# Optimization experiments

Hardware: AMD Instinct MI355X
Metric: run time of the kernel (lower is better)

Reference implementation:

```python
import jax, jax.numpy as jnp
import numpy as np

DIM = 2048
H = 16        # num query heads
HK = 2        # num kv heads
D = DIM // H  # head_dim = 128
G = H // HK   # q heads per kv head = 8
SCALE = 1.0 / np.sqrt(D)


def setup_inputs() -> dict:
    key = jax.random.key(0)
    ks = jax.random.split(key, 9)
    xavier = lambda k, fi, fo: jax.random.uniform(k, (fi, fo), jnp.float32,
                                                  -np.sqrt(6.0 / (fi + fo)), np.sqrt(6.0 / (fi + fo)))
    return {
        "x": jax.random.normal(ks[0], (2, 2048, DIM), jnp.float32),
        "Wq": xavier(ks[1], DIM, H * D),  "bq": jnp.zeros((H * D,), jnp.float32),
        "Wk": xavier(ks[2], DIM, HK * D), "bk": jnp.zeros((HK * D,), jnp.float32),
        "Wv": xavier(ks[3], DIM, HK * D), "bv": jnp.zeros((HK * D,), jnp.float32),
        "Wo": xavier(ks[4], H * D, DIM),  "bo": jnp.zeros((DIM,), jnp.float32),
    }


def reference(x, Wq, bq, Wk, bk, Wv, bv, Wo, bo):
    B, T, C = x.shape
    # projections; q grouped as (kv_head, group) so repeat_interleave becomes a broadcast
    q = (x @ Wq + bq).reshape(B, T, HK, G, D)   # [B,T,Hk,G,D]
    k = (x @ Wk + bk).reshape(B, T, HK, D)      # [B,T,Hk,D]
    v = (x @ Wv + bv).reshape(B, T, HK, D)
    # scores: [B,Hk,G,Tq,Tk] — shared K broadcast across the G query heads per kv head
    scores = jnp.einsum('bqhgd,bshd->bhgqs', q, k) * SCALE
    scores = jnp.clip(scores, -100.0, 100.0)
    attn = jax.nn.softmax(scores, axis=-1)
    out = jnp.einsum('bhgqs,bshd->bqhgd', attn, v).reshape(B, T, H * D)
    return out @ Wo + bo
```

## Files before the change

kernel.cpp:

```cpp
#include <hip/hip_runtime.h>
#include <cstdint>

typedef __bf16 bf16x8 __attribute__((ext_vector_type(8)));
typedef float floatx4 __attribute__((ext_vector_type(4)));
typedef unsigned short u16;
typedef unsigned int u32;

#define SCALE2 0.1275434297677098f
#define CLIP2  144.26950408889634f

__device__ __forceinline__ u16 f2bf(float f) {
  union { float f; u32 i; } v; v.f = f;
  u32 r = v.i + 0x7fffu + ((v.i >> 16) & 1u);
  return (u16)(r >> 16);
}

__device__ __forceinline__ void gll16(const void* g, void* l) {
  __builtin_amdgcn_global_load_lds(
      (const __attribute__((address_space(1))) u32*)g,
      (__attribute__((address_space(3))) u32*)l, 16, 0, 0);
}

__global__ __launch_bounds__(256) void convert_bf16(
    const float* __restrict__ src, u16* __restrict__ dst, int n4) {
  int i = blockIdx.x * 256 + threadIdx.x;
  if (i >= n4) return;
  float4 v = ((const float4*)src)[i];
  ushort4 o;
  o.x = f2bf(v.x); o.y = f2bf(v.y); o.z = f2bf(v.z); o.w = f2bf(v.w);
  ((ushort4*)dst)[i] = o;
}

__global__ __launch_bounds__(256) void transpose_cat(
    const float* __restrict__ W0, const float* __restrict__ W1,
    const float* __restrict__ W2,
    int n1, int n2, int ld0, int ld1, int ld2, int K, u16* __restrict__ Bt) {
  __shared__ u16 tile[32][33];
  const int k0 = blockIdx.x * 32, n0 = blockIdx.y * 32;
  const float* src; int ld, nb;
  if (n0 < n1)      { src = W0; ld = ld0; nb = n0; }
  else if (n0 < n2) { src = W1; ld = ld1; nb = n0 - n1; }
  else              { src = W2; ld = ld2; nb = n0 - n2; }
  const int tx = threadIdx.x, ty = threadIdx.y;
#pragma unroll
  for (int i = 0; i < 4; i++) {
    int k = ty + i * 8;
    tile[k][tx] = f2bf(src[(size_t)(k0 + k) * ld + nb + tx]);
  }
  __syncthreads();
#pragma unroll
  for (int i = 0; i < 4; i++) {
    int n = ty + i * 8;
    Bt[(size_t)(n0 + n) * K + k0 + tx] = tile[tx][n];
  }
}

template <int EPI>
__global__ __launch_bounds__(256) void gemm_bt(
    const u16* __restrict__ A, const u16* __restrict__ Bt,
    const float* __restrict__ bias0, const float* __restrict__ bias1,
    const float* __restrict__ bias2,
    u16* __restrict__ out0, u16* __restrict__ out1, u16* __restrict__ out2,
    float* __restrict__ outf,
    int M, int N, int K) {
  __shared__ u16 As[2][128][32];
  __shared__ u16 Bs[2][128][32];
  const int tid  = threadIdx.x;
  const int w    = tid >> 6, L = tid & 63, ln = L & 15, quad = L >> 4;
  const int m0   = blockIdx.y * 128, n0 = blockIdx.x * 128;
  const int mw   = (w & 1) * 64, nw = (w >> 1) * 64;
  const int sr = w * 32 + (L >> 2), sc = (L & 3) * 8;
  const u16* ga = &A [(size_t)(m0 + sr) * K + sc];
  const u16* gb = &Bt[(size_t)(n0 + sr) * K + sc];
  floatx4 acc[4][4] = {};

  for (int kt = 0; kt < K; kt += 64) {
    __syncthreads();
#pragma unroll
    for (int p = 0; p < 2; p++) {
#pragma unroll
      for (int kh = 0; kh < 2; kh++) {
        gll16(ga + (size_t)(p * 16) * K + kt + kh * 32, &As[kh][w * 32 + p * 16][0]);
        gll16(gb + (size_t)(p * 16) * K + kt + kh * 32, &Bs[kh][w * 32 + p * 16][0]);
      }
    }
    __syncthreads();
#pragma unroll
    for (int kh = 0; kh < 2; kh++) {
      bf16x8 af[4], bf[4];
#pragma unroll
      for (int mb = 0; mb < 4; mb++) af[mb] = *(const bf16x8*)&As[kh][mw + mb * 16 + ln][quad * 8];
#pragma unroll
      for (int nb = 0; nb < 4; nb++) bf[nb] = *(const bf16x8*)&Bs[kh][nw + nb * 16 + ln][quad * 8];
#pragma unroll
      for (int mb = 0; mb < 4; mb++)
#pragma unroll
        for (int nb = 0; nb < 4; nb++)
          acc[mb][nb] = __builtin_amdgcn_mfma_f32_16x16x32_bf16(af[mb], bf[nb], acc[mb][nb], 0, 0, 0);
    }
  }

#pragma unroll
  for (int mb = 0; mb < 4; mb++) {
#pragma unroll
    for (int nb = 0; nb < 4; nb++) {
#pragma unroll
      for (int r = 0; r < 4; r++) {
        const int m = m0 + mw + mb * 16 + quad * 4 + r;
        const int n = n0 + nw + nb * 16 + ln;
        float v = acc[mb][nb][r];
        if constexpr (EPI == 0) {
          if (n < 2048) {
            v = (v + bias0[n]) * SCALE2;
            out0[(size_t)m * 2048 + n] = f2bf(v);
          } else if (n < 2304) {
            const int j = n - 2048;
            v += bias1[j];
            out1[(size_t)m * 256 + j] = f2bf(v);
          } else {
            const int j = n - 2304;
            v += bias2[j];
            const int b = m >> 11, t = m & 2047;
            out2[((size_t)(b * 256 + j)) * 2048 + t] = f2bf(v);
          }
        } else {
          v += bias0[n];
          outf[(size_t)m * (size_t)N + n] = v;
        }
      }
    }
  }
}

__global__ __launch_bounds__(512) void attn_kernel(
    const u16* __restrict__ Q, const u16* __restrict__ K,
    const u16* __restrict__ Vt, u16* __restrict__ O) {
  __shared__ u16 Ksh[16 * 512];
  __shared__ u16 Vsh[16 * 512];
  __shared__ u16 Ps[8][16][72];
  const int tid = threadIdx.x;
  const int w = tid >> 6, L = tid & 63, ln = L & 15, quad = L >> 4;
  const int qt = blockIdx.x, h = blockIdx.y, b = blockIdx.z;
  const int hk = h >> 3;
  const size_t qrow0 = (size_t)b * 2048 + qt * 128 + w * 16;

  const u16* Kbase = K + (size_t)b * 2048 * 256 + hk * 128;
  const u16* Vbase = Vt + (size_t)(b * 2 + hk) * 128 * 2048;

  const int fk0 = w * 2;
  const int kkc0 = fk0 >> 2, knb0 = fk0 & 3;
  const int kkc1 = (fk0 + 1) >> 2, knb1 = (fk0 + 1) & 3;
  const int vkc0 = fk0 >> 3, vnb0 = fk0 & 7;
  const int vkc1 = (fk0 + 1) >> 3, vnb1 = (fk0 + 1) & 7;
  const u16* gK0 = Kbase + (size_t)(knb0 * 16 + ln) * 256 + kkc0 * 32 + quad * 8;
  const u16* gK1 = Kbase + (size_t)(knb1 * 16 + ln) * 256 + kkc1 * 32 + quad * 8;
  const u16* gV0 = Vbase + (size_t)(vnb0 * 16 + ln) * 2048 + vkc0 * 32 + quad * 8;
  const u16* gV1 = Vbase + (size_t)(vnb1 * 16 + ln) * 2048 + vkc1 * 32 + quad * 8;
  u16* lK0 = &Ksh[(size_t)fk0 * 512];
  u16* lK1 = &Ksh[(size_t)(fk0 + 1) * 512];
  u16* lV0 = &Vsh[(size_t)fk0 * 512];
  u16* lV1 = &Vsh[(size_t)(fk0 + 1) * 512];

  bf16x8 qf[4];
#pragma unroll
  for (int kc = 0; kc < 4; kc++)
    qf[kc] = *(const bf16x8*)&Q[(qrow0 + ln) * 2048 + h * 128 + kc * 32 + quad * 8];

  bf16x8 ones;
#pragma unroll
  for (int j = 0; j < 8; j++) {
    union { u16 u; __bf16 bx; } c; c.u = 0x3F80;
    ones[j] = c.bx;
  }

  floatx4 o[8] = {};
  floatx4 o9 = {0.f, 0.f, 0.f, 0.f};
  float mrow[4] = {-1e30f, -1e30f, -1e30f, -1e30f};

  for (int s0 = 0; s0 < 2048; s0 += 64) {
    __syncthreads();
    gll16(gK0 + (size_t)s0 * 256, lK0);
    gll16(gK1 + (size_t)s0 * 256, lK1);
    gll16(gV0 + s0, lV0);
    gll16(gV1 + s0, lV1);
    __syncthreads();

    floatx4 sf[4] = {};
#pragma unroll
    for (int kc = 0; kc < 4; kc++) {
#pragma unroll
      for (int nb = 0; nb < 4; nb++) {
        bf16x8 kf = *(const bf16x8*)&Ksh[(size_t)(kc * 4 + nb) * 512 + L * 8];
        sf[nb] = __builtin_amdgcn_mfma_f32_16x16x32_bf16(qf[kc], kf, sf[nb], 0, 0, 0);
      }
    }
#pragma unroll
    for (int nb = 0; nb < 4; nb++)
#pragma unroll
      for (int r = 0; r < 4; r++)
        sf[nb][r] = __builtin_amdgcn_fmed3f(sf[nb][r], -CLIP2, CLIP2);

    float alpha[4];
#pragma unroll
    for (int r = 0; r < 4; r++) {
      float mx = fmaxf(fmaxf(sf[0][r], sf[1][r]), fmaxf(sf[2][r], sf[3][r]));
#pragma unroll
      for (int off = 1; off < 16; off <<= 1) mx = fmaxf(mx, __shfl_xor(mx, off));
      float mn = fmaxf(mrow[r], mx);
      alpha[r] = __builtin_amdgcn_exp2f(mrow[r] - mn);
      mrow[r] = mn;
    }
    unsigned long long nd = __ballot(alpha[0] < 1.f || alpha[1] < 1.f ||
                                     alpha[2] < 1.f || alpha[3] < 1.f);
    if (nd) {
#pragma unroll
      for (int nb = 0; nb < 8; nb++)
#pragma unroll
        for (int r = 0; r < 4; r++) o[nb][r] *= alpha[r];
#pragma unroll
      for (int r = 0; r < 4; r++) o9[r] *= alpha[r];
    }

#pragma unroll
    for (int nb = 0; nb < 4; nb++)
#pragma unroll
      for (int r = 0; r < 4; r++) {
        float p = __builtin_amdgcn_exp2f(sf[nb][r] - mrow[r]);
        Ps[w][quad * 4 + r][nb * 16 + ln] = f2bf(p);
      }
#pragma unroll
    for (int kc = 0; kc < 2; kc++) {
      bf16x8 pf = *(const bf16x8*)&Ps[w][ln][kc * 32 + quad * 8];
#pragma unroll
      for (int nb = 0; nb < 8; nb++) {
        bf16x8 vf = *(const bf16x8*)&Vsh[(size_t)(kc * 8 + nb) * 512 + L * 8];
        o[nb] = __builtin_amdgcn_mfma_f32_16x16x32_bf16(pf, vf, o[nb], 0, 0, 0);
      }
      o9 = __builtin_amdgcn_mfma_f32_16x16x32_bf16(pf, ones, o9, 0, 0, 0);
    }
  }

#pragma unroll
  for (int r = 0; r < 4; r++) {
    float inv = 1.f / o9[r];
    size_t row = qrow0 + quad * 4 + r;
#pragma unroll
    for (int nb = 0; nb < 8; nb++)
      O[row * 2048 + h * 128 + nb * 16 + ln] = f2bf(o[nb][r] * inv);
  }
}

extern "C" void kernel_launch(void* const* d_in, const int* in_sizes, int n_in,
                              void* d_out, int out_size, void* d_ws, size_t ws_size,
                              hipStream_t stream) {
  const float* x  = (const float*)d_in[0];
  const float* Wq = (const float*)d_in[1];
  const float* bq = (const float*)d_in[2];
  const float* Wk = (const float*)d_in[3];
  const float* bk = (const float*)d_in[4];
  const float* Wv = (const float*)d_in[5];
  const float* bv = (const float*)d_in[6];
  const float* Wo = (const float*)d_in[7];
  const float* bo = (const float*)d_in[8];
  float* out = (float*)d_out;

  char* ws = (char*)d_ws;
  u16* xb     = (u16*)(ws);
  u16* Ob     = (u16*)(ws);
  u16* Wqkv_t = (u16*)(ws + 16777216);
  u16* Wot    = (u16*)(ws + 27262976);
  u16* Qb     = (u16*)(ws + 35651584);
  u16* Kb     = (u16*)(ws + 52428800);
  u16* Vtb    = (u16*)(ws + 54525952);
  (void)in_sizes; (void)n_in; (void)out_size; (void)ws_size;

  convert_bf16<<<8192, 256, 0, stream>>>(x, xb, 2097152);

  transpose_cat<<<dim3(64, 80), dim3(32, 8), 0, stream>>>(
      Wq, Wk, Wv, 2048, 2304, 2048, 256, 256, 2048, Wqkv_t);
  transpose_cat<<<dim3(64, 64), dim3(32, 8), 0, stream>>>(
      Wo, Wo, Wo, 2048, 2048, 2048, 2048, 2048, 2048, Wot);

  gemm_bt<0><<<dim3(20, 32), 256, 0, stream>>>(
      xb, Wqkv_t, bq, bk, bv, Qb, Kb, Vtb, nullptr, 4096, 2560, 2048);

  attn_kernel<<<dim3(16, 16, 2), 512, 0, stream>>>(Qb, Kb, Vtb, Ob);

  gemm_bt<1><<<dim3(16, 32), 256, 0, stream>>>(
      Ob, Wot, bo, nullptr, nullptr, nullptr, nullptr, nullptr, out, 4096, 2048, 2048);
}
```

Measured before the change: 391.0 us.

## Split GEMM K dimension across two wave groups with LDS reduction

The projection GEMMs now launch 512 threads per block. Two groups of four waves each handle half of the K range into separate LDS buffers, and group 1's partial accumulators are reduced into group 0 through shared memory before the epilogue. The aim is more waves per CU to hide load latency, given the small grids (640 and 512 blocks). In exchange each K step does half as much MFMA work per sync, and the epilogue adds four extra barrier-separated LDS reduction rounds.

```diff
diff --git a/kernel.cpp b/kernel.cpp
--- a/kernel.cpp
+++ b/kernel.cpp
@@ -56,7 +56,7 @@
 }
 
 template <int EPI>
-__global__ __launch_bounds__(256) void gemm_bt(
+__global__ __launch_bounds__(512, 4) void gemm_bt(
     const u16* __restrict__ A, const u16* __restrict__ Bt,
     const float* __restrict__ bias0, const float* __restrict__ bias1,
     const float* __restrict__ bias2,
@@ -66,66 +66,77 @@
   __shared__ u16 As[2][128][32];
   __shared__ u16 Bs[2][128][32];
   const int tid  = threadIdx.x;
-  const int w    = tid >> 6, L = tid & 63, ln = L & 15, quad = L >> 4;
+  const int w8   = tid >> 6;
+  const int g    = w8 >> 2;
+  const int w    = w8 & 3;
+  const int L    = tid & 63, ln = L & 15, quad = L >> 4;
   const int m0   = blockIdx.y * 128, n0 = blockIdx.x * 128;
   const int mw   = (w & 1) * 64, nw = (w >> 1) * 64;
-  const int sr = w * 32 + (L >> 2), sc = (L & 3) * 8;
-  const u16* ga = &A [(size_t)(m0 + sr) * K + sc];
-  const u16* gb = &Bt[(size_t)(n0 + sr) * K + sc];
+  const int sr   = w * 32 + (L >> 2), sc = (L & 3) * 8;
+  const int Kh   = K >> 1, kbase = g * Kh;
+  const u16* ga = &A [(size_t)(m0 + sr) * K + kbase + sc];
+  const u16* gb = &Bt[(size_t)(n0 + sr) * K + kbase + sc];
+  u16* la0 = &As[g][w * 32][0];
+  u16* la1 = &As[g][w * 32 + 16][0];
+  u16* lb0 = &Bs[g][w * 32][0];
+  u16* lb1 = &Bs[g][w * 32 + 16][0];
   floatx4 acc[4][4] = {};
 
-  for (int kt = 0; kt < K; kt += 64) {
-    __syncthreads();
-#pragma unroll
-    for (int p = 0; p < 2; p++) {
-#pragma unroll
-      for (int kh = 0; kh < 2; kh++) {
-        gll16(ga + (size_t)(p * 16) * K + kt + kh * 32, &As[kh][w * 32 + p * 16][0]);
-        gll16(gb + (size_t)(p * 16) * K + kt + kh * 32, &Bs[kh][w * 32 + p * 16][0]);
-      }
-    }
-    __syncthreads();
-#pragma unroll
-    for (int kh = 0; kh < 2; kh++) {
-      bf16x8 af[4], bf[4];
-#pragma unroll
-      for (int mb = 0; mb < 4; mb++) af[mb] = *(const bf16x8*)&As[kh][mw + mb * 16 + ln][quad * 8];
-#pragma unroll
-      for (int nb = 0; nb < 4; nb++) bf[nb] = *(const bf16x8*)&Bs[kh][nw + nb * 16 + ln][quad * 8];
-#pragma unroll
-      for (int mb = 0; mb < 4; mb++)
-#pragma unroll
-        for (int nb = 0; nb < 4; nb++)
-          acc[mb][nb] = __builtin_amdgcn_mfma_f32_16x16x32_bf16(af[mb], bf[nb], acc[mb][nb], 0, 0, 0);
-    }
-  }
-
+  for (int kt = 0; kt < Kh; kt += 32) {
+    __syncthreads();
+    gll16(ga + kt, la0);
+    gll16(ga + (size_t)16 * K + kt, la1);
+    gll16(gb + kt, lb0);
+    gll16(gb + (size_t)16 * K + kt, lb1);
+    __syncthreads();
+    bf16x8 af[4], bf[4];
+#pragma unroll
+    for (int mb = 0; mb < 4; mb++) af[mb] = *(const bf16x8*)&As[g][mw + mb * 16 + ln][quad * 8];
+#pragma unroll
+    for (int nb = 0; nb < 4; nb++) bf[nb] = *(const bf16x8*)&Bs[g][nw + nb * 16 + ln][quad * 8];
+#pragma unroll
+    for (int mb = 0; mb < 4; mb++)
+#pragma unroll
+      for (int nb = 0; nb < 4; nb++)
+        acc[mb][nb] = __builtin_amdgcn_mfma_f32_16x16x32_bf16(af[mb], bf[nb], acc[mb][nb], 0, 0, 0);
+  }
+
+  floatx4* cbuf = (floatx4*)&As[0][0][0];
 #pragma unroll
   for (int mb = 0; mb < 4; mb++) {
-#pragma unroll
-    for (int nb = 0; nb < 4; nb++) {
-#pragma unroll
-      for (int r = 0; r < 4; r++) {
-        const int m = m0 + mw + mb * 16 + quad * 4 + r;
-        const int n = n0 + nw + nb * 16 + ln;
-        float v = acc[mb][nb][r];
-        if constexpr (EPI == 0) {
-          if (n < 2048) {
-            v = (v + bias0[n]) * SCALE2;
-            out0[(size_t)m * 2048 + n] = f2bf(v);
-          } else if (n < 2304) {
-            const int j = n - 2048;
-            v += bias1[j];
-            out1[(size_t)m * 256 + j] = f2bf(v);
+    __syncthreads();
+    if (g == 1) {
+#pragma unroll
+      for (int nb = 0; nb < 4; nb++) cbuf[(w * 4 + nb) * 64 + L] = acc[mb][nb];
+    }
+    __syncthreads();
+    if (g == 0) {
+#pragma unroll
+      for (int nb = 0; nb < 4; nb++) {
+        floatx4 other = cbuf[(w * 4 + nb) * 64 + L];
+#pragma unroll
+        for (int r = 0; r < 4; r++) {
+          const int m = m0 + mw + mb * 16 + quad * 4 + r;
+          const int n = n0 + nw + nb * 16 + ln;
+          float v = acc[mb][nb][r] + other[r];
+          if constexpr (EPI == 0) {
+            if (n < 2048) {
+              v = (v + bias0[n]) * SCALE2;
+              out0[(size_t)m * 2048 + n] = f2bf(v);
+            } else if (n < 2304) {
+              const int j = n - 2048;
+              v += bias1[j];
+              out1[(size_t)m * 256 + j] = f2bf(v);
+            } else {
+              const int j = n - 2304;
+              v += bias2[j];
+              const int b = m >> 11, t = m & 2047;
+              out2[((size_t)(b * 256 + j)) * 2048 + t] = f2bf(v);
+            }
           } else {
-            const int j = n - 2304;
-            v += bias2[j];
-            const int b = m >> 11, t = m & 2047;
-            out2[((size_t)(b * 256 + j)) * 2048 + t] = f2bf(v);
+            v += bias0[n];
+            outf[(size_t)m * (size_t)N + n] = v;
           }
-        } else {
-          v += bias0[n];
-          outf[(size_t)m * (size_t)N + n] = v;
         }
       }
     }
@@ -281,11 +292,11 @@
   transpose_cat<<<dim3(64, 64), dim3(32, 8), 0, stream>>>(
       Wo, Wo, Wo, 2048, 2048, 2048, 2048, 2048, 2048, Wot);
 
-  gemm_bt<0><<<dim3(20, 32), 256, 0, stream>>>(
+  gemm_bt<0><<<dim3(20, 32), 512, 0, stream>>>(
       xb, Wqkv_t, bq, bk, bv, Qb, Kb, Vtb, nullptr, 4096, 2560, 2048);
 
   attn_kernel<<<dim3(16, 16, 2), 512, 0, stream>>>(Qb, Kb, Vtb, Ob);
 
-  gemm_bt<1><<<dim3(16, 32), 256, 0, stream>>>(
+  gemm_bt<1><<<dim3(16, 32), 512, 0, stream>>>(
       Ob, Wot, bo, nullptr, nullptr, nullptr, nullptr, nullptr, out, 4096, 2048, 2048);
 }
```

Measured after the change: 389.4 us. No clear change (-0.4%).
